# Optimization experiments

Measured on AMD Instinct MI355X. Metric: run time of the kernel, lower is better.

The kernel has to match this reference:

```python
import jax, jax.numpy as jnp
import numpy as np

B, L, D = 2, 2048, 1024
H, DK, DV = 16, 64, 64
EPS = 1e-6


def setup_inputs() -> dict:
    key = jax.random.key(0)
    ks = jax.random.split(key, 7)
    s = 0.02
    return {
        "x": jax.random.normal(ks[0], (B, L, D), dtype=jnp.float32),
        "Wq": jax.random.normal(ks[1], (D, H * DK), dtype=jnp.float32) * s,
        "Wk": jax.random.normal(ks[2], (D, H * DK), dtype=jnp.float32) * s,
        "Wv": jax.random.normal(ks[3], (D, H * DV), dtype=jnp.float32) * s,
        "Wo": jax.random.normal(ks[4], (H * DV, D), dtype=jnp.float32) * s,
        "ln_gamma": jnp.ones((D,), dtype=jnp.float32),
        "ln_beta": jnp.zeros((D,), dtype=jnp.float32),
    }


def reference(x, Wq, Wk, Wv, Wo, ln_gamma, ln_beta):
    temp = jnp.asarray(DK, x.dtype) ** 0.5
    # projections -> [B, H, L, Dh]
    q = (x @ Wq).reshape(B, L, H, DK).transpose(0, 2, 1, 3)
    k = (x @ Wk).reshape(B, L, H, DK).transpose(0, 2, 1, 3)
    v = (x @ Wv).reshape(B, L, H, DV).transpose(0, 2, 1, 3)
    # naive attention: explicit [B,H,L,L] scores (dropout rate 0 -> identity)
    scores = jnp.einsum("bhqd,bhkd->bhqk", q / temp, k)
    attn = jax.nn.softmax(scores, axis=-1)
    o = jnp.einsum("bhqk,bhkd->bhqd", attn, v)
    o = o.transpose(0, 2, 1, 3).reshape(B, L, H * DV)
    out = o @ Wo + x  # residual
    # LayerNorm(eps=1e-6)
    mu = jnp.mean(out, axis=-1, keepdims=True)
    var = jnp.var(out, axis=-1, keepdims=True)
    return (out - mu) * jax.lax.rsqrt(var + EPS) * ln_gamma + ln_beta
```

## Files before the change

kernel.cpp:

```cpp
#include <hip/hip_runtime.h>


typedef __bf16 bf16;
typedef __bf16 bf16x2 __attribute__((ext_vector_type(2)));
typedef __bf16 bf16x4 __attribute__((ext_vector_type(4)));
typedef __bf16 bf16x8 __attribute__((ext_vector_type(8)));
typedef float floatx4 __attribute__((ext_vector_type(4)));
typedef int intx4 __attribute__((ext_vector_type(4)));

#define MFMA16(a, b, c) __builtin_amdgcn_mfma_f32_16x16x32_bf16((a), (b), (c), 0, 0, 0)

__device__ __forceinline__ void gll16(const bf16* g, bf16* l) {
  __builtin_amdgcn_global_load_lds((const __attribute__((address_space(1))) void*)g,
                                   (__attribute__((address_space(3))) void*)l, 16, 0, 0);
}

__global__ __launch_bounds__(256) void k_prep_x(const float* __restrict__ x, bf16* __restrict__ xb) {
  const int i = (blockIdx.x * 256 + threadIdx.x) * 4;
  const float4 v = *reinterpret_cast<const float4*>(x + i);
  bf16x4 o = {(bf16)v.x, (bf16)v.y, (bf16)v.z, (bf16)v.w};
  *reinterpret_cast<bf16x4*>(xb + i) = o;
}

__global__ __launch_bounds__(256) void k_prep_w(const float* __restrict__ Wq, const float* __restrict__ Wk,
                                                const float* __restrict__ Wv, const float* __restrict__ Wo,
                                                bf16* __restrict__ WT) {
  __shared__ float tile[32][33];
  const int z = blockIdx.z;
  const float* W = (z == 0) ? Wq : (z == 1) ? Wk : (z == 2) ? Wv : Wo;
  const int n0 = blockIdx.x * 32, k0 = blockIdx.y * 32;
  const int tx = threadIdx.x, ty = threadIdx.y;
#pragma unroll
  for (int j = 0; j < 32; j += 8)
    tile[ty + j][tx] = W[(size_t)(k0 + ty + j) * 1024 + n0 + tx];
  __syncthreads();
#pragma unroll
  for (int j = 0; j < 32; j += 8)
    WT[(size_t)(z * 1024 + n0 + ty + j) * 1024 + k0 + tx] = (bf16)tile[tx][ty + j];
}

template <int MODE>
__global__ __launch_bounds__(256) void k_gemm(const bf16* __restrict__ A, const bf16* __restrict__ Bt,
                                              const float* __restrict__ X, float* __restrict__ Y,
                                              bf16* __restrict__ QB, bf16* __restrict__ KB,
                                              bf16* __restrict__ VTB) {
  __shared__ __align__(16) bf16 As[2 * 128 * 64];
  __shared__ __align__(16) bf16 Bs[2 * 128 * 64];
  const int t = threadIdx.x;
  const int lane = t & 63, wv = t >> 6;
  const int qd = lane >> 4, col = lane & 15;
  const int c7 = col & 7;
  const int wm = wv >> 1, wn = wv & 1;
  const int m0 = blockIdx.x * 128, n0 = blockIdx.y * 128;
  const int srow = wv * 8 + (lane >> 3);
  const int scol = ((lane & 7) ^ (lane >> 3)) * 8;
  const bf16* Ag = A + (size_t)(m0 + srow) * 1024 + scol;
  const bf16* Bg = Bt + (size_t)(n0 + srow) * 1024 + scol;

  floatx4 acc[4][4] = {};

#define GSTAGE(ktv, buf)                                                                            \
  do {                                                                                              \
    _Pragma("unroll") for (int rd = 0; rd < 4; rd++) {                                              \
      gll16(Ag + (size_t)rd * 32 * 1024 + (ktv), As + (buf) * 8192 + (rd * 32 + wv * 8) * 64);      \
      gll16(Bg + (size_t)rd * 32 * 1024 + (ktv), Bs + (buf) * 8192 + (rd * 32 + wv * 8) * 64);      \
    }                                                                                               \
  } while (0)

#define GCOMP(buf)                                                                                  \
  do {                                                                                              \
    const bf16* as_ = As + (buf) * 8192;                                                            \
    const bf16* bs_ = Bs + (buf) * 8192;                                                            \
    _Pragma("unroll") for (int ks = 0; ks < 2; ks++) {                                              \
      bf16x8 af[4], bfr[4];                                                                         \
      _Pragma("unroll") for (int i = 0; i < 4; i++)                                                 \
        af[i] = *reinterpret_cast<const bf16x8*>(as_ + (wm * 64 + i * 16 + col) * 64 +              \
                                                 ((ks * 4 + qd) ^ c7) * 8);                         \
      _Pragma("unroll") for (int i = 0; i < 4; i++)                                                 \
        bfr[i] = *reinterpret_cast<const bf16x8*>(bs_ + (wn * 64 + i * 16 + col) * 64 +             \
                                                  ((ks * 4 + qd) ^ c7) * 8);                        \
      _Pragma("unroll") for (int i = 0; i < 4; i++)                                                 \
        _Pragma("unroll") for (int j = 0; j < 4; j++)                                               \
          acc[i][j] = MFMA16(af[i], bfr[j], acc[i][j]);                                             \
    }                                                                                               \
  } while (0)

  GSTAGE(0, 0);
  asm volatile("s_waitcnt vmcnt(0)" ::: "memory");
  __syncthreads();

  for (int kt = 0; kt < 1024; kt += 128) {
    GSTAGE(kt + 64, 1);
    GCOMP(0);
    asm volatile("s_waitcnt vmcnt(0)" ::: "memory");
    __syncthreads();
    if (kt + 128 < 1024) GSTAGE(kt + 128, 0);
    GCOMP(1);
    asm volatile("s_waitcnt vmcnt(0)" ::: "memory");
    __syncthreads();
  }
#undef GSTAGE
#undef GCOMP

#pragma unroll
  for (int i = 0; i < 4; i++) {
#pragma unroll
    for (int j = 0; j < 4; j++) {
      const int mb = m0 + wm * 64 + i * 16 + qd * 4;
      const int n = n0 + wn * 64 + j * 16 + col;
      if (MODE == 0) {
        const int seg = n >> 10;
        const int h = (n & 1023) >> 6, dd = n & 63;
#pragma unroll
        for (int r = 0; r < 4; r++) {
          const int m = mb + r;
          const int bb = m >> 11, l = m & 2047;
          const float v = acc[i][j][r];
          if (seg == 0)
            QB[((size_t)(bb * 16 + h) * 2048 + l) * 64 + dd] = (bf16)(v * 0.18033688f);
          else if (seg == 1)
            KB[((size_t)(bb * 16 + h) * 2048 + l) * 64 + dd] = (bf16)v;
          else
            VTB[((size_t)(bb * 16 + h) * 64 + dd) * 2048 + l] = (bf16)v;
        }
      } else {
#pragma unroll
        for (int r = 0; r < 4; r++) {
          const int m = mb + r;
          Y[(size_t)m * 1024 + n] = acc[i][j][r] + X[(size_t)m * 1024 + n];
        }
      }
    }
  }
}

__global__ __launch_bounds__(256) void k_attn(const bf16* __restrict__ QB, const bf16* __restrict__ KB,
                                              const bf16* __restrict__ VTB, bf16* __restrict__ PO0,
                                              bf16* __restrict__ PO1, float* __restrict__ LS) {
  __shared__ __align__(16) bf16 Ks[2][64 * 64];
  __shared__ __align__(16) bf16 Vs[2][64 * 64];
  const int t = threadIdx.x;
  const int lane = t & 63, wv = t >> 6;
  const int qd = lane >> 4, col = lane & 15;
  const int c7 = col & 7;
  const int bh = blockIdx.y;
  const int z = blockIdx.z;
  const int qr = blockIdx.x * 128 + wv * 32;
  const int lrow0 = wv * 8 + (lane >> 3);
  const int scol = ((lane & 7) ^ (lane >> 3)) * 8;
  const int kg0 = ((lrow0 >> 5) << 5) + (((lrow0 >> 2) & 3) << 3) + (((lrow0 >> 4) & 1) << 2) + (lrow0 & 3);
  const int r1 = lrow0 + 32;
  const int kg1 = ((r1 >> 5) << 5) + (((r1 >> 2) & 3) << 3) + (((r1 >> 4) & 1) << 2) + (r1 & 3);
  const bf16* Kg0 = KB + ((size_t)bh * 2048 + kg0) * 64 + scol;
  const bf16* Kg1 = KB + ((size_t)bh * 2048 + kg1) * 64 + scol;
  const bf16* Vg0 = VTB + ((size_t)bh * 64 + lrow0) * 2048 + scol;
  const bf16* Vg1 = VTB + ((size_t)bh * 64 + lrow0 + 32) * 2048 + scol;

  bf16x8 bQ[2][2];
#pragma unroll
  for (int qt = 0; qt < 2; qt++)
#pragma unroll
    for (int s = 0; s < 2; s++)
      bQ[qt][s] = *reinterpret_cast<const bf16x8*>(QB + ((size_t)bh * 2048 + qr + qt * 16 + col) * 64 + s * 32 + qd * 8);

  floatx4 oacc[2][4] = {};
  float lsum[2] = {0.f, 0.f};
  floatx4 scur[2][4];
  int pk[2][4][2];

#define STAGE(li, ti)                                                  \
  do {                                                                 \
    const int b_ = (li) & 1;                                           \
    gll16(Kg0 + (size_t)(ti) * 4096, &Ks[b_][(wv * 8) * 64]);          \
    gll16(Kg1 + (size_t)(ti) * 4096, &Ks[b_][(32 + wv * 8) * 64]);     \
    gll16(Vg0 + (ti) * 64, &Vs[b_][(wv * 8) * 64]);                    \
    gll16(Vg1 + (ti) * 64, &Vs[b_][(32 + wv * 8) * 64]);               \
  } while (0)

#define QK(li)                                                                                      \
  do {                                                                                              \
    const bf16* ks_ = Ks[(li) & 1];                                                                 \
    _Pragma("unroll") for (int nt = 0; nt < 4; nt++) {                                              \
      bf16x8 a0 = *reinterpret_cast<const bf16x8*>(ks_ + (nt * 16 + col) * 64 + (qd ^ c7) * 8);     \
      bf16x8 a1 = *reinterpret_cast<const bf16x8*>(ks_ + (nt * 16 + col) * 64 + ((4 + qd) ^ c7) * 8); \
      _Pragma("unroll") for (int qt = 0; qt < 2; qt++) {                                            \
        floatx4 zz = {0.f, 0.f, 0.f, 0.f};                                                          \
        zz = MFMA16(a0, bQ[qt][0], zz);                                                             \
        zz = MFMA16(a1, bQ[qt][1], zz);                                                             \
        scur[qt][nt] = zz;                                                                          \
      }                                                                                             \
    }                                                                                               \
  } while (0)

#define EXPPACK()                                                                               \
  do {                                                                                          \
    _Pragma("unroll") for (int qt = 0; qt < 2; qt++) {                                          \
      _Pragma("unroll") for (int nt = 0; nt < 4; nt++) {                                        \
        const float e0 = __builtin_amdgcn_exp2f(scur[qt][nt][0]);                               \
        const float e1 = __builtin_amdgcn_exp2f(scur[qt][nt][1]);                               \
        const float e2 = __builtin_amdgcn_exp2f(scur[qt][nt][2]);                               \
        const float e3 = __builtin_amdgcn_exp2f(scur[qt][nt][3]);                               \
        lsum[qt] += (e0 + e1) + (e2 + e3);                                                      \
        bf16x2 p01, p23;                                                                        \
        p01[0] = (bf16)e0; p01[1] = (bf16)e1;                                                   \
        p23[0] = (bf16)e2; p23[1] = (bf16)e3;                                                   \
        pk[qt][nt][0] = __builtin_bit_cast(int, p01);                                           \
        pk[qt][nt][1] = __builtin_bit_cast(int, p23);                                           \
      }                                                                                         \
    }                                                                                           \
  } while (0)

#define PV(li)                                                                                      \
  do {                                                                                              \
    const bf16* vs_ = Vs[(li) & 1];                                                                 \
    bf16x8 bV[4][2];                                                                                \
    _Pragma("unroll") for (int nd = 0; nd < 4; nd++) {                                              \
      bV[nd][0] = *reinterpret_cast<const bf16x8*>(vs_ + (nd * 16 + col) * 64 + (qd ^ c7) * 8);     \
      bV[nd][1] = *reinterpret_cast<const bf16x8*>(vs_ + (nd * 16 + col) * 64 + ((4 + qd) ^ c7) * 8); \
    }                                                                                               \
    _Pragma("unroll") for (int qt = 0; qt < 2; qt++) {                                              \
      _Pragma("unroll") for (int s = 0; s < 2; s++) {                                               \
        intx4 w;                                                                                    \
        w[0] = pk[qt][2 * s][0]; w[1] = pk[qt][2 * s][1];                                           \
        w[2] = pk[qt][2 * s + 1][0]; w[3] = pk[qt][2 * s + 1][1];                                   \
        const bf16x8 aP = __builtin_bit_cast(bf16x8, w);                                            \
        _Pragma("unroll") for (int nd = 0; nd < 4; nd++)                                            \
          oacc[qt][nd] = MFMA16(aP, bV[nd][s], oacc[qt][nd]);                                       \
      }                                                                                             \
    }                                                                                               \
  } while (0)

  const int t0 = z * 16;
  STAGE(0, t0);
  __syncthreads();
  QK(0);
  for (int ii = 1; ii < 16; ii++) {
    __syncthreads();
    STAGE(ii, t0 + ii);
    EXPPACK();
    PV(ii - 1);
    __syncthreads();
    QK(ii);
  }
  EXPPACK();
  PV(15);

#pragma unroll
  for (int qt = 0; qt < 2; qt++) {
    lsum[qt] += __shfl_xor(lsum[qt], 16);
    lsum[qt] += __shfl_xor(lsum[qt], 32);
  }
  if (qd == 0) {
#pragma unroll
    for (int qt = 0; qt < 2; qt++)
      LS[(size_t)z * 65536 + (size_t)bh * 2048 + qr + qt * 16 + col] = lsum[qt];
  }
  bf16* PO = z ? PO1 : PO0;
  const int bb = bh >> 4, h = bh & 15;
#pragma unroll
  for (int qt = 0; qt < 2; qt++) {
#pragma unroll
    for (int r = 0; r < 4; r++) {
      const size_t m = (size_t)bb * 2048 + qr + qt * 16 + qd * 4 + r;
#pragma unroll
      for (int nd = 0; nd < 4; nd++)
        PO[m * 1024 + h * 64 + nd * 16 + col] = (bf16)(oacc[qt][nd][r]);
    }
  }
#undef STAGE
#undef QK
#undef EXPPACK
#undef PV
}

__global__ __launch_bounds__(256) void k_comb(const bf16* __restrict__ PO0, const bf16* __restrict__ PO1,
                                              const float* __restrict__ LS, bf16* __restrict__ OB) {
  const size_t idx = ((size_t)blockIdx.x * 256 + threadIdx.x) * 4;
  const int m = (int)(idx >> 10), c = (int)(idx & 1023);
  const int bb = m >> 11, l = m & 2047, h = c >> 6;
  const int bh = bb * 16 + h;
  const float linv = 1.f / (LS[(size_t)bh * 2048 + l] + LS[65536 + (size_t)bh * 2048 + l]);
  const bf16x4 a = *reinterpret_cast<const bf16x4*>(PO0 + idx);
  const bf16x4 b = *reinterpret_cast<const bf16x4*>(PO1 + idx);
  bf16x4 o;
#pragma unroll
  for (int i = 0; i < 4; i++) o[i] = (bf16)(((float)a[i] + (float)b[i]) * linv);
  *reinterpret_cast<bf16x4*>(OB + idx) = o;
}

__global__ __launch_bounds__(256) void k_ln(const float* __restrict__ Yin, const float* __restrict__ gamma,
                                            const float* __restrict__ beta, float* __restrict__ out) {
  __shared__ float red[8];
  const int row = blockIdx.x, t = threadIdx.x;
  const float4 v = *reinterpret_cast<const float4*>(Yin + (size_t)row * 1024 + t * 4);
  float s = v.x + v.y + v.z + v.w;
  float ss = v.x * v.x + v.y * v.y + v.z * v.z + v.w * v.w;
#pragma unroll
  for (int d = 1; d < 64; d <<= 1) {
    s += __shfl_xor(s, d);
    ss += __shfl_xor(ss, d);
  }
  if ((t & 63) == 0) {
    red[t >> 6] = s;
    red[4 + (t >> 6)] = ss;
  }
  __syncthreads();
  s = red[0] + red[1] + red[2] + red[3];
  ss = red[4] + red[5] + red[6] + red[7];
  const float mu = s * (1.f / 1024.f);
  const float var = ss * (1.f / 1024.f) - mu * mu;
  const float rs = rsqrtf(var + 1e-6f);
  const float4 g = *reinterpret_cast<const float4*>(gamma + t * 4);
  const float4 bt = *reinterpret_cast<const float4*>(beta + t * 4);
  float4 o;
  o.x = (v.x - mu) * rs * g.x + bt.x;
  o.y = (v.y - mu) * rs * g.y + bt.y;
  o.z = (v.z - mu) * rs * g.z + bt.z;
  o.w = (v.w - mu) * rs * g.w + bt.w;
  *reinterpret_cast<float4*>(out + (size_t)row * 1024 + t * 4) = o;
}

extern "C" void kernel_launch(void* const* d_in, const int* in_sizes, int n_in,
                              void* d_out, int out_size, void* d_ws, size_t ws_size,
                              hipStream_t stream) {
  (void)in_sizes; (void)n_in; (void)out_size; (void)ws_size;
  const float* x = (const float*)d_in[0];
  const float* Wq = (const float*)d_in[1];
  const float* Wk = (const float*)d_in[2];
  const float* Wv = (const float*)d_in[3];
  const float* Wo = (const float*)d_in[4];
  const float* gamma = (const float*)d_in[5];
  const float* beta = (const float*)d_in[6];

  char* ws = (char*)d_ws;
  const size_t MB = 1ull << 20;
  bf16* XB = (bf16*)(ws);
  bf16* PO0 = (bf16*)(ws);
  bf16* OB = (bf16*)(ws);
  bf16* WT = (bf16*)(ws + 8 * MB);
  bf16* QB = (bf16*)(ws + 16 * MB);
  bf16* KB = (bf16*)(ws + 24 * MB);
  bf16* VTB = (bf16*)(ws + 32 * MB);
  bf16* PO1 = (bf16*)(ws + 40 * MB);
  float* LS = (float*)(ws + 48 * MB);
  float* Y = (float*)(ws + 16 * MB);

  k_prep_x<<<4096, 256, 0, stream>>>(x, XB);
  k_prep_w<<<dim3(32, 32, 4), dim3(32, 8), 0, stream>>>(Wq, Wk, Wv, Wo, WT);
  k_gemm<0><<<dim3(32, 24), 256, 0, stream>>>(XB, WT, nullptr, nullptr, QB, KB, VTB);
  k_attn<<<dim3(16, 32, 2), 256, 0, stream>>>(QB, KB, VTB, PO0, PO1, LS);
  k_comb<<<4096, 256, 0, stream>>>(PO0, PO1, LS, OB);
  k_gemm<1><<<dim3(32, 8), 256, 0, stream>>>(OB, WT + (size_t)3072 * 1024, x, Y,
                                             nullptr, nullptr, nullptr);
  k_ln<<<4096, 256, 0, stream>>>(Y, gamma, beta, (float*)d_out);
}
```

Before: 222.9 us.

## Triple-buffer K/V tiles in attention with explicit vmcnt waits and raw barriers

The attention kernel moves from double to triple buffering of K and V tiles in LDS, prefetching two tiles ahead. The loop is unrolled by three with rotating buffer indices. It replaces __syncthreads with an explicit s_waitcnt vmcnt(4) plus s_barrier, so one tile's loads can stay in flight during compute. The aim is to hide global-to-LDS load latency behind MFMA work. In exchange, LDS use rises by half, which may lower occupancy, and the tail issues redundant clamped loads.

```diff
diff --git a/kernel.cpp b/kernel.cpp
--- a/kernel.cpp
+++ b/kernel.cpp
@@ -137,8 +137,8 @@
 __global__ __launch_bounds__(256) void k_attn(const bf16* __restrict__ QB, const bf16* __restrict__ KB,
                                               const bf16* __restrict__ VTB, bf16* __restrict__ PO0,
                                               bf16* __restrict__ PO1, float* __restrict__ LS) {
-  __shared__ __align__(16) bf16 Ks[2][64 * 64];
-  __shared__ __align__(16) bf16 Vs[2][64 * 64];
+  __shared__ __align__(16) bf16 Ks[3][64 * 64];
+  __shared__ __align__(16) bf16 Vs[3][64 * 64];
   const int t = threadIdx.x;
   const int lane = t & 63, wv = t >> 6;
   const int qd = lane >> 4, col = lane & 15;
@@ -168,18 +168,17 @@
   floatx4 scur[2][4];
   int pk[2][4][2];
 
-#define STAGE(li, ti)                                                  \
+#define STAGE(bu, ti)                                                  \
   do {                                                                 \
-    const int b_ = (li) & 1;                                           \
-    gll16(Kg0 + (size_t)(ti) * 4096, &Ks[b_][(wv * 8) * 64]);          \
-    gll16(Kg1 + (size_t)(ti) * 4096, &Ks[b_][(32 + wv * 8) * 64]);     \
-    gll16(Vg0 + (ti) * 64, &Vs[b_][(wv * 8) * 64]);                    \
-    gll16(Vg1 + (ti) * 64, &Vs[b_][(32 + wv * 8) * 64]);               \
-  } while (0)
-
-#define QK(li)                                                                                      \
+    gll16(Kg0 + (size_t)(ti) * 4096, &Ks[bu][(wv * 8) * 64]);          \
+    gll16(Kg1 + (size_t)(ti) * 4096, &Ks[bu][(32 + wv * 8) * 64]);     \
+    gll16(Vg0 + (ti) * 64, &Vs[bu][(wv * 8) * 64]);                    \
+    gll16(Vg1 + (ti) * 64, &Vs[bu][(32 + wv * 8) * 64]);               \
+  } while (0)
+
+#define QK(bu)                                                                                      \
   do {                                                                                              \
-    const bf16* ks_ = Ks[(li) & 1];                                                                 \
+    const bf16* ks_ = Ks[bu];                                                                       \
     _Pragma("unroll") for (int nt = 0; nt < 4; nt++) {                                              \
       bf16x8 a0 = *reinterpret_cast<const bf16x8*>(ks_ + (nt * 16 + col) * 64 + (qd ^ c7) * 8);     \
       bf16x8 a1 = *reinterpret_cast<const bf16x8*>(ks_ + (nt * 16 + col) * 64 + ((4 + qd) ^ c7) * 8); \
@@ -210,9 +209,9 @@
     }                                                                                           \
   } while (0)
 
-#define PV(li)                                                                                      \
+#define PV(bu)                                                                                      \
   do {                                                                                              \
-    const bf16* vs_ = Vs[(li) & 1];                                                                 \
+    const bf16* vs_ = Vs[bu];                                                                       \
     bf16x8 bV[4][2];                                                                                \
     _Pragma("unroll") for (int nd = 0; nd < 4; nd++) {                                              \
       bV[nd][0] = *reinterpret_cast<const bf16x8*>(vs_ + (nd * 16 + col) * 64 + (qd ^ c7) * 8);     \
@@ -230,20 +229,32 @@
     }                                                                                               \
   } while (0)
 
+#define ITER(cur, prv, ti)                                             \
+  do {                                                                 \
+    asm volatile("s_waitcnt vmcnt(4)" ::: "memory");                   \
+    __builtin_amdgcn_s_barrier();                                      \
+    EXPPACK();                                                         \
+    QK(cur);                                                           \
+    PV(prv);                                                           \
+    __builtin_amdgcn_s_barrier();                                      \
+    STAGE(prv, ((ti) + 2 <= t0 + 15) ? ((ti) + 2) : (t0 + 15));        \
+  } while (0)
+
   const int t0 = z * 16;
   STAGE(0, t0);
-  __syncthreads();
+  STAGE(1, t0 + 1);
+  asm volatile("s_waitcnt vmcnt(4)" ::: "memory");
+  __builtin_amdgcn_s_barrier();
   QK(0);
-  for (int ii = 1; ii < 16; ii++) {
-    __syncthreads();
-    STAGE(ii, t0 + ii);
-    EXPPACK();
-    PV(ii - 1);
-    __syncthreads();
-    QK(ii);
+  __builtin_amdgcn_s_barrier();
+  STAGE(2, t0 + 2);
+  for (int j = 1; j < 16; j += 3) {
+    ITER(1, 0, t0 + j);
+    ITER(2, 1, t0 + j + 1);
+    ITER(0, 2, t0 + j + 2);
   }
   EXPPACK();
-  PV(15);
+  PV(0);
 
 #pragma unroll
   for (int qt = 0; qt < 2; qt++) {
@@ -271,6 +282,7 @@
 #undef QK
 #undef EXPPACK
 #undef PV
+#undef ITER
 }
 
 __global__ __launch_bounds__(256) void k_comb(const bf16* __restrict__ PO0, const bf16* __restrict__ PO1,
```

New measurement: 215.3 us. -3.4%, faster.
